# Kernel tuning notes

Hardware: AMD Instinct MI355X
Metric: run time of the kernel (lower is better)

The kernel has to match this reference:

```python
import jax, jax.numpy as jnp
import numpy as np

BATCH = 32768
NUM_CLASSES = 1000

def setup_inputs() -> dict:
    key = jax.random.key(0)
    k1, k2 = jax.random.split(key)
    input = jax.random.normal(k1, (BATCH, NUM_CLASSES), dtype=jnp.float32)
    target = jax.random.randint(k2, (BATCH, NUM_CLASSES), 0, 2, dtype=jnp.int32)
    return {"input": input, "target": target}

def reference(input, target):
    # LSEP: loss = log(1 + sum_{i} sum_{p in pos_i} sum_{n in neg_i} exp(x[i,n] - x[i,p]))
    # The pair sum factorizes per sample:
    #   sum_{p,n} exp(x_n - x_p) = (sum_{n in neg} exp(x_n)) * (sum_{p in pos} exp(-x_p))
    pos = target > 0
    neg = target == 0
    s_neg = jnp.sum(jnp.where(neg, jnp.exp(input), 0.0), axis=1)   # [B]
    s_pos = jnp.sum(jnp.where(pos, jnp.exp(-input), 0.0), axis=1)  # [B]
    total = jnp.sum(s_neg * s_pos)
    return jnp.log1p(total).reshape(1).astype(jnp.float32)
```

## Files before the change

kernel.cpp:

```cpp
#include <hip/hip_runtime.h>
#include <math.h>

#define BATCH   32768
#define NCLS    1000
#define NC4     250
#define NBLOCKS 2048
#define NWAVES  (NBLOCKS * 4)

__global__ __launch_bounds__(256) void lsep_row_kernel(
    const float* __restrict__ x,
    const int*   __restrict__ t,
    float* __restrict__ wave_out) {

    const int tid   = threadIdx.x;
    const int lane  = tid & 63;
    const int gwave = blockIdx.x * 4 + (tid >> 6);

    float acc = 0.0f;

    #pragma unroll
    for (int r = 0; r < BATCH / NWAVES; ++r) {
        const int row = gwave + r * NWAVES;
        const float4* xr = (const float4*)(x + (size_t)row * NCLS);
        const int4*   tr = (const int4*)(t + (size_t)row * NCLS);

        float4 xv[4];
        int4   tv[4];
        #pragma unroll
        for (int j = 0; j < 4; ++j) {
            const int idx = lane + 64 * j;
            if (idx < NC4) {
                xv[j] = xr[idx];
                tv[j] = tr[idx];
            }
        }

        float sn = 0.0f, sp = 0.0f;
        #pragma unroll
        for (int j = 0; j < 4; ++j) {
            const int idx = lane + 64 * j;
            if (idx < NC4) {
                {   float e = __expf(xv[j].x); float r1 = __builtin_amdgcn_rcpf(e);
                    if (tv[j].x == 0) sn += e; else sp += r1; }
                {   float e = __expf(xv[j].y); float r1 = __builtin_amdgcn_rcpf(e);
                    if (tv[j].y == 0) sn += e; else sp += r1; }
                {   float e = __expf(xv[j].z); float r1 = __builtin_amdgcn_rcpf(e);
                    if (tv[j].z == 0) sn += e; else sp += r1; }
                {   float e = __expf(xv[j].w); float r1 = __builtin_amdgcn_rcpf(e);
                    if (tv[j].w == 0) sn += e; else sp += r1; }
            }
        }

        #pragma unroll
        for (int off = 32; off > 0; off >>= 1) {
            sn += __shfl_down(sn, off, 64);
            sp += __shfl_down(sp, off, 64);
        }

        if (lane == 0) acc += sn * sp;
    }

    if (lane == 0) wave_out[gwave] = acc;
}

__global__ __launch_bounds__(256) void lsep_reduce_kernel(
    const float* __restrict__ wave_out,
    float* __restrict__ out) {

    const int tid = threadIdx.x;
    const float4* r4 = (const float4*)wave_out;

    float4 a[8];
    #pragma unroll
    for (int j = 0; j < 8; ++j)
        a[j] = r4[tid + 256 * j];

    float v = 0.0f;
    #pragma unroll
    for (int j = 0; j < 8; ++j)
        v += (a[j].x + a[j].y) + (a[j].z + a[j].w);

    #pragma unroll
    for (int off = 32; off > 0; off >>= 1)
        v += __shfl_down(v, off, 64);

    __shared__ float sv[4];
    const int wave = tid >> 6;
    const int lane = tid & 63;
    if (lane == 0) sv[wave] = v;
    __syncthreads();

    if (tid == 0) {
        float total = (sv[0] + sv[1]) + (sv[2] + sv[3]);
        out[0] = log1pf(total);
    }
}

extern "C" void kernel_launch(void* const* d_in, const int* in_sizes, int n_in,
                              void* d_out, int out_size, void* d_ws, size_t ws_size,
                              hipStream_t stream) {
    const float* x = (const float*)d_in[0];
    const int*   t = (const int*)d_in[1];
    float* out     = (float*)d_out;
    float* wave_ws = (float*)d_ws;

    lsep_row_kernel<<<NBLOCKS, 256, 0, stream>>>(x, t, wave_ws);
    lsep_reduce_kernel<<<1, 256, 0, stream>>>(wave_ws, out);
}
```

Baseline: 270.1 us.

## Use DPP wave reductions, branchless exp selection, and clamped unconditional loads

```diff
diff --git a/kernel.cpp b/kernel.cpp
--- a/kernel.cpp
+++ b/kernel.cpp
@@ -6,8 +6,30 @@
 #define NC4     250
 #define NBLOCKS 2048
 #define NWAVES  (NBLOCKS * 4)
+#define RPW     (BATCH / NWAVES)
 
-__global__ __launch_bounds__(256) void lsep_row_kernel(
+__device__ __forceinline__ float wave_sum_dpp(float v) {
+    int x;
+    x = __builtin_amdgcn_update_dpp(0, __float_as_int(v), 0x111, 0xf, 0xf, true);
+    v += __int_as_float(x);
+    x = __builtin_amdgcn_update_dpp(0, __float_as_int(v), 0x112, 0xf, 0xf, true);
+    v += __int_as_float(x);
+    x = __builtin_amdgcn_update_dpp(0, __float_as_int(v), 0x114, 0xf, 0xf, true);
+    v += __int_as_float(x);
+    x = __builtin_amdgcn_update_dpp(0, __float_as_int(v), 0x118, 0xf, 0xf, true);
+    v += __int_as_float(x);
+    x = __builtin_amdgcn_update_dpp(0, __float_as_int(v), 0x142, 0xa, 0xf, true);
+    v += __int_as_float(x);
+    x = __builtin_amdgcn_update_dpp(0, __float_as_int(v), 0x143, 0xc, 0xf, true);
+    v += __int_as_float(x);
+    return v;
+}
+
+__device__ __forceinline__ float bcast63(float v) {
+    return __int_as_float(__builtin_amdgcn_readlane(__float_as_int(v), 63));
+}
+
+__global__ __launch_bounds__(256, 4) void lsep_row_kernel(
     const float* __restrict__ x,
     const int*   __restrict__ t,
     float* __restrict__ wave_out) {
@@ -19,7 +41,7 @@
     float acc = 0.0f;
 
     #pragma unroll
-    for (int r = 0; r < BATCH / NWAVES; ++r) {
+    for (int r = 0; r < RPW; ++r) {
         const int row = gwave + r * NWAVES;
         const float4* xr = (const float4*)(x + (size_t)row * NCLS);
         const int4*   tr = (const int4*)(t + (size_t)row * NCLS);
@@ -29,38 +51,39 @@
         #pragma unroll
         for (int j = 0; j < 4; ++j) {
             const int idx = lane + 64 * j;
-            if (idx < NC4) {
-                xv[j] = xr[idx];
-                tv[j] = tr[idx];
-            }
+            const int ci  = idx < NC4 ? idx : NC4 - 1;
+            xv[j] = xr[ci];
+            tv[j] = tr[ci];
         }
 
         float sn = 0.0f, sp = 0.0f;
         #pragma unroll
         for (int j = 0; j < 4; ++j) {
-            const int idx = lane + 64 * j;
-            if (idx < NC4) {
-                {   float e = __expf(xv[j].x); float r1 = __builtin_amdgcn_rcpf(e);
-                    if (tv[j].x == 0) sn += e; else sp += r1; }
-                {   float e = __expf(xv[j].y); float r1 = __builtin_amdgcn_rcpf(e);
-                    if (tv[j].y == 0) sn += e; else sp += r1; }
-                {   float e = __expf(xv[j].z); float r1 = __builtin_amdgcn_rcpf(e);
-                    if (tv[j].z == 0) sn += e; else sp += r1; }
-                {   float e = __expf(xv[j].w); float r1 = __builtin_amdgcn_rcpf(e);
-                    if (tv[j].w == 0) sn += e; else sp += r1; }
-            }
+            const bool valid = (lane + 64 * j) < NC4;
+            {   const bool isneg = tv[j].x == 0;
+                float v = __expf(isneg ? xv[j].x : -xv[j].x);
+                sn += (valid && isneg)  ? v : 0.0f;
+                sp += (valid && !isneg) ? v : 0.0f; }
+            {   const bool isneg = tv[j].y == 0;
+                float v = __expf(isneg ? xv[j].y : -xv[j].y);
+                sn += (valid && isneg)  ? v : 0.0f;
+                sp += (valid && !isneg) ? v : 0.0f; }
+            {   const bool isneg = tv[j].z == 0;
+                float v = __expf(isneg ? xv[j].z : -xv[j].z);
+                sn += (valid && isneg)  ? v : 0.0f;
+                sp += (valid && !isneg) ? v : 0.0f; }
+            {   const bool isneg = tv[j].w == 0;
+                float v = __expf(isneg ? xv[j].w : -xv[j].w);
+                sn += (valid && isneg)  ? v : 0.0f;
+                sp += (valid && !isneg) ? v : 0.0f; }
         }
 
-        #pragma unroll
-        for (int off = 32; off > 0; off >>= 1) {
-            sn += __shfl_down(sn, off, 64);
-            sp += __shfl_down(sp, off, 64);
-        }
-
-        if (lane == 0) acc += sn * sp;
+        const float SP = bcast63(wave_sum_dpp(sp));
+        acc += sn * SP;
     }
 
-    if (lane == 0) wave_out[gwave] = acc;
+    const float tot = wave_sum_dpp(acc);
+    if (lane == 63) wave_out[gwave] = tot;
 }
 
 __global__ __launch_bounds__(256) void lsep_reduce_kernel(
```

After: 273.0 us. No clear change (+1.1%).
